# Kernel tuning notes

Measured on AMD Instinct MI355X. Metric: run time of the kernel, lower is better.

## Reference

```python
import jax, jax.numpy as jnp
import numpy as np

NEG_INF = -9e15  # matches -9000000000000000.0 in torch code
ALPHA = 0.2      # LeakyReLU negative slope


def setup_inputs() -> dict:
    key = jax.random.key(0)
    k1, k2, k3, k4 = jax.random.split(key, 4)
    B, N, Fin, Fout = 8, 2048, 256, 256
    h = jax.random.normal(k1, (B, N, Fin), dtype=jnp.float32)
    adj = jax.random.randint(k2, (B, N, N), 0, 2, dtype=jnp.int32)
    W = jax.random.normal(k3, (Fin, Fout), dtype=jnp.float32) * 0.05
    a = jax.random.normal(k4, (2 * Fout, 1), dtype=jnp.float32) * 0.05
    return {"h": h, "adj": adj, "W": W, "a": a}


def reference(h, adj, W, a):
    # h: [B,N,Fin], adj: [B,N,N], W: [Fin,Fout], a: [2*Fout,1]
    Fout = W.shape[1]
    Wh = jnp.matmul(h, W)                       # [B,N,Fout]
    # Decompose concat-based additive score: e_ij = LReLU(a1.Wh_i + a2.Wh_j)
    a1 = a[:Fout, 0]                            # source-node part
    a2 = a[Fout:, 0]                            # target-node part
    s1 = jnp.einsum('bnf,f->bn', Wh, a1)        # [B,N]
    s2 = jnp.einsum('bnf,f->bn', Wh, a2)        # [B,N]
    e = jax.nn.leaky_relu(s1[:, :, None] + s2[:, None, :], negative_slope=ALPHA)  # [B,N,N]
    attn = jnp.where(adj > 0, e, NEG_INF)
    attn = jax.nn.softmax(attn, axis=2)          # masked softmax over neighbors
    # dropout omitted (deterministic eval-mode reference)
    h_prime = jnp.matmul(attn, Wh)               # [B,N,Fout]
    return h_prime
```

## Files before the change

kernel.cpp:

```cpp
#include <hip/hip_runtime.h>
#include <cstdint>

#define ALPHA 0.2f

constexpr int NB = 8;
constexpr int NN = 2048;
constexpr int NF = 256;

typedef __attribute__((ext_vector_type(8))) short bf16x8;
typedef __attribute__((ext_vector_type(4))) float f32x4;

__device__ __forceinline__ float bf2f(unsigned short u) {
    union { unsigned int i; float f; } v;
    v.i = ((unsigned int)u) << 16;
    return v.f;
}
__device__ __forceinline__ unsigned short f2bf(float f) {
    union { float f; unsigned int i; } v;
    v.f = f;
    v.i += 0x7fffu + ((v.i >> 16) & 1);
    return (unsigned short)(v.i >> 16);
}

__global__ __launch_bounds__(256) void k_wt(const float* __restrict__ W,
                                            unsigned short* __restrict__ WT,
                                            float* __restrict__ s1,
                                            float* __restrict__ s2) {
    const int t = threadIdx.x;
    const int gid = blockIdx.x * 256 + t;
    s1[gid] = 0.f;
    s2[gid] = 0.f;
    const int k = blockIdx.x * 4 + (t >> 6);
    const int f0 = (t & 63) * 4;
    const float4 w = *(const float4*)&W[k * NF + f0];
    WT[(f0 + 0) * NF + k] = f2bf(w.x);
    WT[(f0 + 1) * NF + k] = f2bf(w.y);
    WT[(f0 + 2) * NF + k] = f2bf(w.z);
    WT[(f0 + 3) * NF + k] = f2bf(w.w);
}

__global__ __launch_bounds__(256, 4) void k_wh(const float* __restrict__ h,
                                               const unsigned short* __restrict__ WT,
                                               const float* __restrict__ a,
                                               unsigned short* __restrict__ WhT,
                                               float* __restrict__ s1,
                                               float* __restrict__ s2) {
    __shared__ __align__(16) unsigned short As[64][72];
    __shared__ __align__(16) unsigned short Bs[64][72];
    const int tid = threadIdx.x;
    const int lane = tid & 63;
    const int l16 = lane & 15;
    const int quad = lane >> 4;
    const int wave = tid >> 6;

    const int p = blockIdx.x;
    const int xcd = p & 7;
    const int q = p >> 3;
    const int rowTile = xcd + (q >> 2) * 8;
    const int row0 = rowTile * 64;
    const int col0 = (q & 3) * 64;

    const int bb = row0 >> 11;
    const int n0 = row0 & (NN - 1);
    const int mb = (wave & 1) * 32;
    const int nb = (wave >> 1) * 32;

    f32x4 acc[2][2];
#pragma unroll
    for (int mf = 0; mf < 2; ++mf)
#pragma unroll
        for (int nf = 0; nf < 2; ++nf) acc[mf][nf] = (f32x4){0.f, 0.f, 0.f, 0.f};

    const int r0 = tid >> 4;
    const int k4 = (tid & 15) * 4;
    const int f0w = tid >> 3;
    const int k8 = (tid & 7) * 8;

    const float* hP = &h[(size_t)(row0 + r0) * NF + k4];
    const unsigned short* wP = &WT[(size_t)(col0 + f0w) * NF + k8];

    float4 h0, h1, h2, h3;
    uint4 wv0, wv1;

#define LOADW(K0)                                                      \
    do {                                                               \
        h0 = *(const float4*)&hP[(size_t)(0 * 16) * NF + (K0)];        \
        h1 = *(const float4*)&hP[(size_t)(1 * 16) * NF + (K0)];        \
        h2 = *(const float4*)&hP[(size_t)(2 * 16) * NF + (K0)];        \
        h3 = *(const float4*)&hP[(size_t)(3 * 16) * NF + (K0)];        \
        wv0 = *(const uint4*)&wP[(K0)];                                \
        wv1 = *(const uint4*)&wP[(size_t)32 * NF + (K0)];              \
    } while (0)

    LOADW(0);

    for (int k0 = 0; k0 < NF; k0 += 64) {
        ushort4 o;
        o.x = f2bf(h0.x); o.y = f2bf(h0.y); o.z = f2bf(h0.z); o.w = f2bf(h0.w);
        *(ushort4*)&As[r0 + 0][k4] = o;
        o.x = f2bf(h1.x); o.y = f2bf(h1.y); o.z = f2bf(h1.z); o.w = f2bf(h1.w);
        *(ushort4*)&As[r0 + 16][k4] = o;
        o.x = f2bf(h2.x); o.y = f2bf(h2.y); o.z = f2bf(h2.z); o.w = f2bf(h2.w);
        *(ushort4*)&As[r0 + 32][k4] = o;
        o.x = f2bf(h3.x); o.y = f2bf(h3.y); o.z = f2bf(h3.z); o.w = f2bf(h3.w);
        *(ushort4*)&As[r0 + 48][k4] = o;
        *(uint4*)&Bs[f0w][k8] = wv0;
        *(uint4*)&Bs[f0w + 32][k8] = wv1;
        __syncthreads();
        if (k0 + 64 < NF) LOADW(k0 + 64);
#pragma unroll
        for (int ks = 0; ks < 64; ks += 32) {
            bf16x8 av[2], bv[2];
#pragma unroll
            for (int mf = 0; mf < 2; ++mf)
                av[mf] = *(const bf16x8*)&As[mb + mf * 16 + l16][ks + quad * 8];
#pragma unroll
            for (int nf = 0; nf < 2; ++nf)
                bv[nf] = *(const bf16x8*)&Bs[nb + nf * 16 + l16][ks + quad * 8];
#pragma unroll
            for (int mf = 0; mf < 2; ++mf)
#pragma unroll
                for (int nf = 0; nf < 2; ++nf)
                    acc[mf][nf] = __builtin_amdgcn_mfma_f32_16x16x32_bf16(
                        av[mf], bv[nf], acc[mf][nf], 0, 0, 0);
        }
        __syncthreads();
    }
#undef LOADW

#pragma unroll
    for (int mf = 0; mf < 2; ++mf) {
#pragma unroll
        for (int nf = 0; nf < 2; ++nf) {
            const size_t f = col0 + nb + nf * 16 + l16;
            const int nr = n0 + mb + mf * 16 + quad * 4;
            ushort4 o;
            o.x = f2bf(acc[mf][nf][0]);
            o.y = f2bf(acc[mf][nf][1]);
            o.z = f2bf(acc[mf][nf][2]);
            o.w = f2bf(acc[mf][nf][3]);
            *(ushort4*)&WhT[((size_t)bb * NF + f) * NN + nr] = o;
        }
    }

    float a1v[2], a2v[2];
#pragma unroll
    for (int nf = 0; nf < 2; ++nf) {
        const int f = col0 + nb + nf * 16 + l16;
        a1v[nf] = a[f];
        a2v[nf] = a[NF + f];
    }
#pragma unroll
    for (int mf = 0; mf < 2; ++mf) {
#pragma unroll
        for (int r = 0; r < 4; ++r) {
            float p1 = acc[mf][0][r] * a1v[0] + acc[mf][1][r] * a1v[1];
            float p2 = acc[mf][0][r] * a2v[0] + acc[mf][1][r] * a2v[1];
            p1 += __shfl_xor(p1, 1); p2 += __shfl_xor(p2, 1);
            p1 += __shfl_xor(p1, 2); p2 += __shfl_xor(p2, 2);
            p1 += __shfl_xor(p1, 4); p2 += __shfl_xor(p2, 4);
            p1 += __shfl_xor(p1, 8); p2 += __shfl_xor(p2, 8);
            if (l16 == 0) {
                const int n = n0 + mb + mf * 16 + quad * 4 + r;
                atomicAdd(&s1[bb * NN + n], p1);
                atomicAdd(&s2[bb * NN + n], p2);
            }
        }
    }
}

__global__ __launch_bounds__(512, 2) void k_attn(const unsigned short* __restrict__ WhT,
                                                 const int* __restrict__ adj,
                                                 const float* __restrict__ s1g,
                                                 const float* __restrict__ s2g,
                                                 float* __restrict__ out) {
    __shared__ __align__(16) unsigned short WhsT[256][72];
    __shared__ __align__(16) unsigned short Pb[64][72];
    __shared__ float s1_s[64];
    __shared__ float l_s[64];

    const int tid = threadIdx.x;
    const int lane = tid & 63;
    const int l16 = lane & 15;
    const int quad = lane >> 4;
    const int wave = tid >> 6;
    const int bb = blockIdx.x & 7;
    const int i0 = (blockIdx.x >> 3) * 64;

    if (tid < 64) {
        s1_s[tid] = s1g[bb * NN + i0 + tid];
        l_s[tid] = 0.f;
    }
    __syncthreads();

    f32x4 acc[4][2];
#pragma unroll
    for (int m = 0; m < 4; ++m)
#pragma unroll
        for (int nf = 0; nf < 2; ++nf) acc[m][nf] = (f32x4){0.f, 0.f, 0.f, 0.f};

    const size_t whtBase = (size_t)bb * NF * NN;
    const size_t adjBase = (size_t)bb * NN * NN;
    const float* s2b = s2g + bb * NN;

    const int whF = tid >> 3;
    const int whK = (tid & 7) * 8;
    const int pIr = tid >> 4;
    const int pKq = (tid & 15) * 4;

    const unsigned short* whP = &WhT[whtBase + (size_t)whF * NN + whK];
    const int* adjP0 = &adj[adjBase + (size_t)(i0 + pIr) * NN + pKq];
    const int* adjP1 = adjP0 + 32 * NN;
    const float* s2P = &s2b[pKq];

    uint4 w0, w1, w2, w3;
    int4 am0, am1;
    float4 sv0;

#define LOAD_TILE(J0)                                                         \
    do {                                                                      \
        const int j0_ = (J0);                                                 \
        w0 = *(const uint4*)&whP[(size_t)(0 * 64) * NN + j0_];                \
        w1 = *(const uint4*)&whP[(size_t)(1 * 64) * NN + j0_];                \
        w2 = *(const uint4*)&whP[(size_t)(2 * 64) * NN + j0_];                \
        w3 = *(const uint4*)&whP[(size_t)(3 * 64) * NN + j0_];                \
        am0 = *(const int4*)&adjP0[j0_];                                      \
        am1 = *(const int4*)&adjP1[j0_];                                      \
        sv0 = *(const float4*)&s2P[j0_];                                      \
    } while (0)

    LOAD_TILE(0);

    for (int t = 0; t < NN / 64; ++t) {
        *(uint4*)&WhsT[whF + 0 * 64][whK] = w0;
        *(uint4*)&WhsT[whF + 1 * 64][whK] = w1;
        *(uint4*)&WhsT[whF + 2 * 64][whK] = w2;
        *(uint4*)&WhsT[whF + 3 * 64][whK] = w3;
#pragma unroll
        for (int it = 0; it < 2; ++it) {
            const int ir = pIr + it * 32;
            const int4 av = it ? am1 : am0;
            const float s1v = s1_s[ir];
            float x0 = s1v + sv0.x, x1 = s1v + sv0.y;
            float x2 = s1v + sv0.z, x3 = s1v + sv0.w;
            x0 = x0 > 0.f ? x0 : ALPHA * x0;
            x1 = x1 > 0.f ? x1 : ALPHA * x1;
            x2 = x2 > 0.f ? x2 : ALPHA * x2;
            x3 = x3 > 0.f ? x3 : ALPHA * x3;
            const float p0 = av.x > 0 ? __expf(x0) : 0.f;
            const float p1 = av.y > 0 ? __expf(x1) : 0.f;
            const float p2 = av.z > 0 ? __expf(x2) : 0.f;
            const float p3 = av.w > 0 ? __expf(x3) : 0.f;
            uint2 pk;
            pk.x = (unsigned int)f2bf(p0) | ((unsigned int)f2bf(p1) << 16);
            pk.y = (unsigned int)f2bf(p2) | ((unsigned int)f2bf(p3) << 16);
            *(uint2*)&Pb[ir][pKq] = pk;
            float ps = (p0 + p1) + (p2 + p3);
            ps += __shfl_xor(ps, 8);
            ps += __shfl_xor(ps, 4);
            ps += __shfl_xor(ps, 2);
            ps += __shfl_xor(ps, 1);
            if ((tid & 15) == 0) l_s[ir] += ps;
        }
        __syncthreads();
        if (t + 1 < NN / 64) LOAD_TILE((t + 1) * 64);
        const int f0 = wave * 32;
#pragma unroll
        for (int k0 = 0; k0 < 64; k0 += 32) {
            bf16x8 af[4];
#pragma unroll
            for (int m = 0; m < 4; ++m)
                af[m] = *(const bf16x8*)&Pb[m * 16 + l16][k0 + quad * 8];
#pragma unroll
            for (int nf = 0; nf < 2; ++nf) {
                const bf16x8 bfr =
                    *(const bf16x8*)&WhsT[f0 + nf * 16 + l16][k0 + quad * 8];
#pragma unroll
                for (int m = 0; m < 4; ++m)
                    acc[m][nf] = __builtin_amdgcn_mfma_f32_16x16x32_bf16(
                        af[m], bfr, acc[m][nf], 0, 0, 0);
            }
        }
        __syncthreads();
    }
#undef LOAD_TILE

    if (tid < 64) l_s[tid] = 1.0f / l_s[tid];
    __syncthreads();

    const int f0 = wave * 32;
#pragma unroll
    for (int m = 0; m < 4; ++m) {
#pragma unroll
        for (int r = 0; r < 4; ++r) {
            const int row = m * 16 + quad * 4 + r;
            const float inv = l_s[row];
#pragma unroll
            for (int nf = 0; nf < 2; ++nf) {
                out[((size_t)bb * NN + i0 + row) * NF + f0 + nf * 16 + l16] =
                    acc[m][nf][r] * inv;
            }
        }
    }
}

extern "C" void kernel_launch(void* const* d_in, const int* in_sizes, int n_in,
                              void* d_out, int out_size, void* d_ws, size_t ws_size,
                              hipStream_t stream) {
    const float* h = (const float*)d_in[0];
    const int* adj = (const int*)d_in[1];
    const float* W = (const float*)d_in[2];
    const float* a = (const float*)d_in[3];
    float* out = (float*)d_out;

    unsigned short* WhT = (unsigned short*)d_ws;
    float* s1 = (float*)((char*)d_ws + (size_t)NB * NN * NF * sizeof(unsigned short));
    float* s2 = s1 + (size_t)NB * NN;
    unsigned short* WT = (unsigned short*)(s2 + (size_t)NB * NN);

    k_wt<<<dim3(64), dim3(256), 0, stream>>>(W, WT, s1, s2);
    k_wh<<<dim3((NB * NN / 64) * (NF / 64)), dim3(256), 0, stream>>>(h, WT, a, WhT, s1, s2);
    k_attn<<<dim3(NB * (NN / 64)), dim3(512), 0, stream>>>(WhT, adj, s1, s2, out);
}
```

Measured before the change: 256.6 us.

## Split attention kernel across feature halves and load Wh fragments directly from global

The attention kernel now uses 32-row blocks of 256 threads, and each block covers half of the 256 output features. That quadruples the grid, so more waves can be resident per CU. The Wh operand is no longer staged through shared memory: each wave loads its MFMA B-fragments straight from global memory, which removes the large LDS tile and its writes. In exchange, the adjacency rows and the exp/softmax weights are read and computed twice (once per feature half), and more Wh traffic has to be served from L2.

Measured after the change: 263.9 us. 2.8% more time.

```diff
diff --git a/kernel.cpp b/kernel.cpp
--- a/kernel.cpp
+++ b/kernel.cpp
@@ -169,15 +169,14 @@
     }
 }
 
-__global__ __launch_bounds__(512, 2) void k_attn(const unsigned short* __restrict__ WhT,
+__global__ __launch_bounds__(256, 4) void k_attn(const unsigned short* __restrict__ WhT,
                                                  const int* __restrict__ adj,
                                                  const float* __restrict__ s1g,
                                                  const float* __restrict__ s2g,
                                                  float* __restrict__ out) {
-    __shared__ __align__(16) unsigned short WhsT[256][72];
-    __shared__ __align__(16) unsigned short Pb[64][72];
-    __shared__ float s1_s[64];
-    __shared__ float l_s[64];
+    __shared__ __align__(16) unsigned short Pb[32][72];
+    __shared__ float s1_s[32];
+    __shared__ float l_s[32];
 
     const int tid = threadIdx.x;
     const int lane = tid & 63;
@@ -185,60 +184,45 @@
     const int quad = lane >> 4;
     const int wave = tid >> 6;
     const int bb = blockIdx.x & 7;
-    const int i0 = (blockIdx.x >> 3) * 64;
-
-    if (tid < 64) {
+    const int rest = blockIdx.x >> 3;
+    const int i0 = (rest >> 1) * 32;
+    const int fbase = (rest & 1) * 128 + wave * 32;
+
+    if (tid < 32) {
         s1_s[tid] = s1g[bb * NN + i0 + tid];
         l_s[tid] = 0.f;
     }
     __syncthreads();
 
-    f32x4 acc[4][2];
-#pragma unroll
-    for (int m = 0; m < 4; ++m)
+    f32x4 acc[2][2];
+#pragma unroll
+    for (int m = 0; m < 2; ++m)
 #pragma unroll
         for (int nf = 0; nf < 2; ++nf) acc[m][nf] = (f32x4){0.f, 0.f, 0.f, 0.f};
 
     const size_t whtBase = (size_t)bb * NF * NN;
     const size_t adjBase = (size_t)bb * NN * NN;
-    const float* s2b = s2g + bb * NN;
-
-    const int whF = tid >> 3;
-    const int whK = (tid & 7) * 8;
+
     const int pIr = tid >> 4;
     const int pKq = (tid & 15) * 4;
-
-    const unsigned short* whP = &WhT[whtBase + (size_t)whF * NN + whK];
     const int* adjP0 = &adj[adjBase + (size_t)(i0 + pIr) * NN + pKq];
-    const int* adjP1 = adjP0 + 32 * NN;
-    const float* s2P = &s2b[pKq];
-
-    uint4 w0, w1, w2, w3;
+    const int* adjP1 = adjP0 + 16 * NN;
+    const float* s2P = &s2g[bb * NN + pKq];
+
+    const unsigned short* whB0 = &WhT[whtBase + (size_t)(fbase + l16) * NN + quad * 8];
+    const unsigned short* whB1 = whB0 + (size_t)16 * NN;
+
     int4 am0, am1;
     float4 sv0;
-
-#define LOAD_TILE(J0)                                                         \
-    do {                                                                      \
-        const int j0_ = (J0);                                                 \
-        w0 = *(const uint4*)&whP[(size_t)(0 * 64) * NN + j0_];                \
-        w1 = *(const uint4*)&whP[(size_t)(1 * 64) * NN + j0_];                \
-        w2 = *(const uint4*)&whP[(size_t)(2 * 64) * NN + j0_];                \
-        w3 = *(const uint4*)&whP[(size_t)(3 * 64) * NN + j0_];                \
-        am0 = *(const int4*)&adjP0[j0_];                                      \
-        am1 = *(const int4*)&adjP1[j0_];                                      \
-        sv0 = *(const float4*)&s2P[j0_];                                      \
-    } while (0)
-
-    LOAD_TILE(0);
+    am0 = *(const int4*)&adjP0[0];
+    am1 = *(const int4*)&adjP1[0];
+    sv0 = *(const float4*)&s2P[0];
 
     for (int t = 0; t < NN / 64; ++t) {
-        *(uint4*)&WhsT[whF + 0 * 64][whK] = w0;
-        *(uint4*)&WhsT[whF + 1 * 64][whK] = w1;
-        *(uint4*)&WhsT[whF + 2 * 64][whK] = w2;
-        *(uint4*)&WhsT[whF + 3 * 64][whK] = w3;
+        const int j0 = t * 64;
 #pragma unroll
         for (int it = 0; it < 2; ++it) {
-            const int ir = pIr + it * 32;
+            const int ir = pIr + it * 16;
             const int4 av = it ? am1 : am0;
             const float s1v = s1_s[ir];
             float x0 = s1v + sv0.x, x1 = s1v + sv0.y;
@@ -262,42 +246,53 @@
             ps += __shfl_xor(ps, 1);
             if ((tid & 15) == 0) l_s[ir] += ps;
         }
+        const uint4 b00 = *(const uint4*)&whB0[j0];
+        const uint4 b01 = *(const uint4*)&whB0[j0 + 32];
+        const uint4 b10 = *(const uint4*)&whB1[j0];
+        const uint4 b11 = *(const uint4*)&whB1[j0 + 32];
         __syncthreads();
-        if (t + 1 < NN / 64) LOAD_TILE((t + 1) * 64);
-        const int f0 = wave * 32;
-#pragma unroll
-        for (int k0 = 0; k0 < 64; k0 += 32) {
-            bf16x8 af[4];
-#pragma unroll
-            for (int m = 0; m < 4; ++m)
-                af[m] = *(const bf16x8*)&Pb[m * 16 + l16][k0 + quad * 8];
-#pragma unroll
-            for (int nf = 0; nf < 2; ++nf) {
-                const bf16x8 bfr =
-                    *(const bf16x8*)&WhsT[f0 + nf * 16 + l16][k0 + quad * 8];
-#pragma unroll
-                for (int m = 0; m < 4; ++m)
-                    acc[m][nf] = __builtin_amdgcn_mfma_f32_16x16x32_bf16(
-                        af[m], bfr, acc[m][nf], 0, 0, 0);
-            }
+        if (t + 1 < NN / 64) {
+            am0 = *(const int4*)&adjP0[j0 + 64];
+            am1 = *(const int4*)&adjP1[j0 + 64];
+            sv0 = *(const float4*)&s2P[j0 + 64];
+        }
+        {
+            bf16x8 a0 = *(const bf16x8*)&Pb[l16][quad * 8];
+            bf16x8 a1 = *(const bf16x8*)&Pb[16 + l16][quad * 8];
+            acc[0][0] = __builtin_amdgcn_mfma_f32_16x16x32_bf16(
+                a0, *(const bf16x8*)&b00, acc[0][0], 0, 0, 0);
+            acc[1][0] = __builtin_amdgcn_mfma_f32_16x16x32_bf16(
+                a1, *(const bf16x8*)&b00, acc[1][0], 0, 0, 0);
+            acc[0][1] = __builtin_amdgcn_mfma_f32_16x16x32_bf16(
+                a0, *(const bf16x8*)&b10, acc[0][1], 0, 0, 0);
+            acc[1][1] = __builtin_amdgcn_mfma_f32_16x16x32_bf16(
+                a1, *(const bf16x8*)&b10, acc[1][1], 0, 0, 0);
+            a0 = *(const bf16x8*)&Pb[l16][32 + quad * 8];
+            a1 = *(const bf16x8*)&Pb[16 + l16][32 + quad * 8];
+            acc[0][0] = __builtin_amdgcn_mfma_f32_16x16x32_bf16(
+                a0, *(const bf16x8*)&b01, acc[0][0], 0, 0, 0);
+            acc[1][0] = __builtin_amdgcn_mfma_f32_16x16x32_bf16(
+                a1, *(const bf16x8*)&b01, acc[1][0], 0, 0, 0);
+            acc[0][1] = __builtin_amdgcn_mfma_f32_16x16x32_bf16(
+                a0, *(const bf16x8*)&b11, acc[0][1], 0, 0, 0);
+            acc[1][1] = __builtin_amdgcn_mfma_f32_16x16x32_bf16(
+                a1, *(const bf16x8*)&b11, acc[1][1], 0, 0, 0);
         }
         __syncthreads();
     }
-#undef LOAD_TILE
-
-    if (tid < 64) l_s[tid] = 1.0f / l_s[tid];
+
+    if (tid < 32) l_s[tid] = 1.0f / l_s[tid];
     __syncthreads();
 
-    const int f0 = wave * 32;
-#pragma unroll
-    for (int m = 0; m < 4; ++m) {
+#pragma unroll
+    for (int m = 0; m < 2; ++m) {
 #pragma unroll
         for (int r = 0; r < 4; ++r) {
             const int row = m * 16 + quad * 4 + r;
             const float inv = l_s[row];
 #pragma unroll
             for (int nf = 0; nf < 2; ++nf) {
-                out[((size_t)bb * NN + i0 + row) * NF + f0 + nf * 16 + l16] =
+                out[((size_t)bb * NN + i0 + row) * NF + fbase + nf * 16 + l16] =
                     acc[m][nf][r] * inv;
             }
         }
@@ -320,5 +315,5 @@
 
     k_wt<<<dim3(64), dim3(256), 0, stream>>>(W, WT, s1, s2);
     k_wh<<<dim3((NB * NN / 64) * (NF / 64)), dim3(256), 0, stream>>>(h, WT, a, WhT, s1, s2);
-    k_attn<<<dim3(NB * (NN / 64)), dim3(512), 0, stream>>>(WhT, adj, s1, s2, out);
-}
+    k_attn<<<dim3(NB * (NN / 32) * 2), dim3(256), 0, stream>>>(WhT, adj, s1, s2, out);
+}
```
